# Kernel optimization log

Hardware: AMD Instinct MI355X
Metric: run time of the kernel (lower is better)

Reference implementation:

```python
import jax, jax.numpy as jnp
import numpy as np

B, C, H, W = 32, 256, 56, 56
EPS = 1e-5

def _bin_act(x):
    # ReActNet BinaryActivation: forward = sign(x), STE via piecewise polynomial
    out1 = jnp.where(x < -1.0, -1.0, x * x + 2.0 * x)
    out2 = jnp.where(x < 0.0, out1, -x * x + 2.0 * x)
    out3 = jnp.where(x < 1.0, out2, 1.0)
    return out3 + jax.lax.stop_gradient(jnp.sign(x) - out3)

def _bin_weight(w):
    # forward = sign(w) * mean(|w|) per out-channel; grad via clip(w,-1,1)
    scale = jnp.mean(jnp.abs(w), axis=(1, 2, 3), keepdims=True)
    bw = jnp.sign(w) * scale
    cl = jnp.clip(w, -1.0, 1.0)
    return cl + jax.lax.stop_gradient(bw - cl)

def _conv1x1(x, w):
    # x: [B,C,H,W], w: [P,C,1,1] -> [B,P,H,W]
    return jnp.einsum('bchw,pc->bphw', x, w[:, :, 0, 0])

def _shift(x, k):
    # chunk channels into 4, roll H+k, H-k, W+k, W-k (circular, as torch.roll)
    x1, x2, x3, x4 = jnp.split(x, 4, axis=1)
    return jnp.concatenate([
        jnp.roll(x1, k, axis=2), jnp.roll(x2, -k, axis=2),
        jnp.roll(x3, k, axis=3), jnp.roll(x4, -k, axis=3)], axis=1)

def setup_inputs() -> dict:
    key = jax.random.key(0)
    ks = jax.random.split(key, 8)
    return {
        'x': jax.random.normal(ks[0], (B, C, H, W), dtype=jnp.float32),
        'bias0': jax.random.normal(ks[1], (C,), dtype=jnp.float32) * 0.1,
        'w1': jax.random.normal(ks[2], (C, C, 1, 1), dtype=jnp.float32) * 0.05,
        'w2': jax.random.normal(ks[3], (C, C, 1, 1), dtype=jnp.float32) * 0.05,
        'w3': jax.random.normal(ks[4], (C, C, 1, 1), dtype=jnp.float32) * 0.05,
        'gamma': jnp.ones((C,), dtype=jnp.float32),
        'beta': jnp.zeros((C,), dtype=jnp.float32),
        'bias1': jax.random.normal(ks[5], (C,), dtype=jnp.float32) * 0.1,
        'alpha': jnp.full((C,), 0.25, dtype=jnp.float32),  # PReLU init
        'bias2': jax.random.normal(ks[6], (C,), dtype=jnp.float32) * 0.1,
    }

def reference(x, bias0, w1, w2, w3, gamma, beta, bias1, alpha, bias2):
    ch = lambda v: v[None, :, None, None]
    residual = x
    out = x + ch(bias0)                      # move0 (LearnableBias)
    a = _bin_act(out)                        # binary activation (sign, STE)
    o1 = _conv1x1(a, _bin_weight(w1))        # binary_conv
    o2 = _conv1x1(_shift(a, 1), _bin_weight(w2))   # Shift + binary_conv1
    o3 = _conv1x1(_shift(a, 3), _bin_weight(w3))   # GlobalShift + binary_conv2
    s = o1 + o2 + o3
    # BatchNorm (training mode: batch statistics over B,H,W)
    mean = jnp.mean(s, axis=(0, 2, 3))
    var = jnp.var(s, axis=(0, 2, 3))
    h = (s - ch(mean)) * jax.lax.rsqrt(ch(var) + EPS) * ch(gamma) + ch(beta)
    h = h + residual                          # residual add
    h = h + ch(bias1)                         # move1
    h = jnp.where(h >= 0, h, ch(alpha) * h)   # PReLU
    h = h + ch(bias2)                         # move2
    return h
```

## Files before the change

kernel.cpp:

```cpp
#include <hip/hip_runtime.h>

typedef unsigned int u32;
typedef int i32x4 __attribute__((ext_vector_type(4)));
typedef float f32x4 __attribute__((ext_vector_type(4)));

#define HWP  3136
#define NPOS 100352
#define NMBLK 1568

#define ACT_OFF 0ull
#define ACT_BYTES (25690112ull)
#define W8_OFF  (ACT_OFF + ACT_BYTES)
#define W8_BYTES (196608ull)
#define SC_OFF  (W8_OFF + W8_BYTES)
#define SC_BYTES (3072ull)
#define PS_OFF  (SC_OFF + SC_BYTES)
#define PS_BYTES (256ull * NMBLK * 4)
#define PQ_OFF  (PS_OFF + PS_BYTES)
#define PQ_BYTES (256ull * NMBLK * 4)
#define PAR_OFF (PQ_OFF + PQ_BYTES)

__global__ __launch_bounds__(64) void k_pack_w(
    const float* __restrict__ w1, const float* __restrict__ w2,
    const float* __restrict__ w3, signed char* __restrict__ w8,
    float* __restrict__ scales) {
  int bid = blockIdx.x;
  int conv = bid >> 8, p = bid & 255;
  const float* w = (conv == 0) ? w1 : (conv == 1) ? w2 : w3;
  int lane = threadIdx.x;
  float asum = 0.0f;
#pragma unroll
  for (int k = 0; k < 4; ++k) {
    float v = w[p * 256 + k * 64 + lane];
    asum += fabsf(v);
    w8[(size_t)(conv * 256 + p) * 256 + k * 64 + lane] =
        (v > 0.0f) ? (signed char)1 : (signed char)-1;
  }
#pragma unroll
  for (int off = 32; off > 0; off >>= 1) asum += __shfl_down(asum, off);
  if (lane == 0) scales[conv * 256 + p] = asum * (1.0f / 256.0f);
}

__global__ __launch_bounds__(256) void k_pack_a(
    const float* __restrict__ x, const float* __restrict__ bias0,
    i32x4* __restrict__ act16) {
  int pos = blockIdx.x * 256 + threadIdx.x;
  int b = pos / HWP;
  int hw = pos - b * HWP;
  const float* xp = x + (size_t)b * 256 * HWP + hw;
  i32x4* op = act16 + (size_t)pos * 16;
#pragma unroll 2
  for (int c16 = 0; c16 < 16; ++c16) {
    i32x4 vv;
#pragma unroll
    for (int q = 0; q < 4; ++q) {
      u32 bb = 0;
#pragma unroll
      for (int cc = 0; cc < 4; ++cc) {
        int c = c16 * 16 + q * 4 + cc;
        float v = xp[(size_t)c * HWP] + bias0[c];
        bb |= (u32)((v > 0.0f) ? 0x01u : 0xFFu) << (cc * 8);
      }
      vv[q] = (int)bb;
    }
    op[c16] = vv;
  }
}

__device__ __forceinline__ void compute_s(
    int m, int n0, const signed char* __restrict__ act,
    const signed char* __restrict__ w8, const float* __restrict__ scales,
    signed char* lds, f32x4 (&sout)[4]) {
  const int tid = threadIdx.x;
  const int lane = tid & 63, wid = tid >> 6;
  const int l15 = lane & 15, l4 = lane >> 4;
  const int ch = n0 + wid * 16 + l15;

  i32x4 bfrag[3][4];
#pragma unroll
  for (int conv = 0; conv < 3; ++conv)
#pragma unroll
    for (int ks = 0; ks < 4; ++ks)
      bfrag[conv][ks] = *(const i32x4*)(w8 + (size_t)(conv * 256 + ch) * 256 +
                                        ks * 64 + l4 * 16);
  float sc0 = scales[ch], sc1 = scales[256 + ch], sc2 = scales[512 + ch];

  int bimg = m / 49;
  int hw0 = (m - bimg * 49) * 64;
  for (int id = tid; id < 3072; id += 512) {
    int tile = id >> 10;
    int rem = id & 1023;
    int row = rem >> 4;
    int c16 = rem & 15;
    int grp = c16 >> 2;
    int hw = hw0 + row;
    int h = hw / 56, w = hw - h * 56;
    int sh = h, sw = w;
    if (tile == 1) {
      if (grp == 0)      sh = (h == 0) ? 55 : h - 1;
      else if (grp == 1) sh = (h == 55) ? 0 : h + 1;
      else if (grp == 2) sw = (w == 0) ? 55 : w - 1;
      else               sw = (w == 55) ? 0 : w + 1;
    } else if (tile == 2) {
      if (grp == 0)      sh = (h < 3) ? h + 53 : h - 3;
      else if (grp == 1) sh = (h >= 53) ? h - 53 : h + 3;
      else if (grp == 2) sw = (w < 3) ? w + 53 : w - 3;
      else               sw = (w >= 53) ? w - 53 : w + 3;
    }
    size_t spos = (size_t)(bimg * HWP + sh * 56 + sw);
    i32x4 v = *(const i32x4*)(act + spos * 256 + c16 * 16);
    *(i32x4*)(lds + tile * 16384 + row * 256 + ((c16 ^ (row & 7)) << 4)) = v;
  }
  __syncthreads();

#pragma unroll
  for (int msub = 0; msub < 4; ++msub) {
    int row = msub * 16 + l15;
    int rx = row & 7;
    i32x4 acc0 = {0, 0, 0, 0}, acc1 = {0, 0, 0, 0}, acc2 = {0, 0, 0, 0};
#pragma unroll
    for (int ks = 0; ks < 4; ++ks) {
      int off = row * 256 + (((ks * 4 + l4) ^ rx) << 4);
      i32x4 a0 = *(const i32x4*)(lds + off);
      i32x4 a1 = *(const i32x4*)(lds + 16384 + off);
      i32x4 a2 = *(const i32x4*)(lds + 32768 + off);
      acc0 = __builtin_amdgcn_mfma_i32_16x16x64_i8(a0, bfrag[0][ks], acc0, 0, 0, 0);
      acc1 = __builtin_amdgcn_mfma_i32_16x16x64_i8(a1, bfrag[1][ks], acc1, 0, 0, 0);
      acc2 = __builtin_amdgcn_mfma_i32_16x16x64_i8(a2, bfrag[2][ks], acc2, 0, 0, 0);
    }
    f32x4 s;
#pragma unroll
    for (int r = 0; r < 4; ++r)
      s[r] = sc0 * (float)acc0[r] + sc1 * (float)acc1[r] + sc2 * (float)acc2[r];
    sout[msub] = s;
  }
}

__global__ __launch_bounds__(512) void k_stats2(
    const signed char* __restrict__ act, const signed char* __restrict__ w8,
    const float* __restrict__ scales, float* __restrict__ ps,
    float* __restrict__ pq) {
  __shared__ alignas(16) signed char lds[49152];
  int m = blockIdx.x, n0 = blockIdx.y * 128;
  f32x4 s[4];
  compute_s(m, n0, act, w8, scales, lds, s);
  float ss = 0.0f, sq = 0.0f;
#pragma unroll
  for (int msub = 0; msub < 4; ++msub)
#pragma unroll
    for (int r = 0; r < 4; ++r) {
      ss += s[msub][r];
      sq = fmaf(s[msub][r], s[msub][r], sq);
    }
  ss += __shfl_xor(ss, 16); sq += __shfl_xor(sq, 16);
  ss += __shfl_xor(ss, 32); sq += __shfl_xor(sq, 32);
  int lane = threadIdx.x & 63, wid = threadIdx.x >> 6;
  if ((lane >> 4) == 0) {
    int ch = n0 + wid * 16 + lane;
    ps[(size_t)ch * NMBLK + m] = ss;
    pq[(size_t)ch * NMBLK + m] = sq;
  }
}

__global__ __launch_bounds__(256) void k_bn(
    const float* __restrict__ ps, const float* __restrict__ pq,
    const float* __restrict__ gamma, const float* __restrict__ beta,
    const float* __restrict__ bias1, float* __restrict__ par) {
  int ch = blockIdx.x;
  int tid = threadIdx.x;
  double as = 0.0, aq = 0.0;
  for (int i = tid; i < NMBLK; i += 256) {
    as += (double)ps[(size_t)ch * NMBLK + i];
    aq += (double)pq[(size_t)ch * NMBLK + i];
  }
  __shared__ double sd0[256], sd1[256];
  sd0[tid] = as; sd1[tid] = aq;
  __syncthreads();
  for (int s = 128; s > 0; s >>= 1) {
    if (tid < s) { sd0[tid] += sd0[tid + s]; sd1[tid] += sd1[tid + s]; }
    __syncthreads();
  }
  if (tid == 0) {
    double mean = sd0[0] * (1.0 / NPOS);
    double var = sd1[0] * (1.0 / NPOS) - mean * mean;
    float mm = (float)((double)gamma[ch] / sqrt(var + 1e-5));
    par[ch] = mm;
    par[256 + ch] = beta[ch] + bias1[ch] - (float)mean * mm;
  }
}

__global__ __launch_bounds__(512) void k_out2(
    const signed char* __restrict__ act, const signed char* __restrict__ w8,
    const float* __restrict__ scales, const float* __restrict__ par,
    const float* __restrict__ alpha, const float* __restrict__ bias2,
    const float* __restrict__ x, float* __restrict__ out) {
  __shared__ alignas(16) signed char lds[49152];
  int m = blockIdx.x, n0 = blockIdx.y * 128;
  f32x4 s[4];
  compute_s(m, n0, act, w8, scales, lds, s);
  int tid = threadIdx.x, lane = tid & 63, wid = tid >> 6;
  int l15 = lane & 15, l4 = lane >> 4;
  int ch = n0 + wid * 16 + l15;
  float mul = par[ch], add = par[256 + ch], al = alpha[ch], b2 = bias2[ch];
  int bimg = m / 49;
  int hw0 = (m - bimg * 49) * 64;
  size_t base = ((size_t)bimg * 256 + ch) * HWP + hw0 + l4 * 4;
#pragma unroll
  for (int msub = 0; msub < 4; ++msub) {
    f32x4 xv = *(const f32x4*)(x + base + msub * 16);
    f32x4 o;
#pragma unroll
    for (int r = 0; r < 4; ++r) {
      float t = fmaf(s[msub][r], mul, add) + xv[r];
      t = (t >= 0.0f) ? t : al * t;
      o[r] = t + b2;
    }
    *(f32x4*)(out + base + msub * 16) = o;
  }
}

extern "C" void kernel_launch(void* const* d_in, const int* in_sizes, int n_in,
                              void* d_out, int out_size, void* d_ws,
                              size_t ws_size, hipStream_t stream) {
  const float* x     = (const float*)d_in[0];
  const float* bias0 = (const float*)d_in[1];
  const float* w1    = (const float*)d_in[2];
  const float* w2    = (const float*)d_in[3];
  const float* w3    = (const float*)d_in[4];
  const float* gamma = (const float*)d_in[5];
  const float* beta  = (const float*)d_in[6];
  const float* bias1 = (const float*)d_in[7];
  const float* alpha = (const float*)d_in[8];
  const float* bias2 = (const float*)d_in[9];
  float* out = (float*)d_out;

  char* ws = (char*)d_ws;
  signed char* act = (signed char*)(ws + ACT_OFF);
  i32x4* act16     = (i32x4*)(ws + ACT_OFF);
  signed char* w8  = (signed char*)(ws + W8_OFF);
  float* scales    = (float*)(ws + SC_OFF);
  float* ps        = (float*)(ws + PS_OFF);
  float* pq        = (float*)(ws + PQ_OFF);
  float* par       = (float*)(ws + PAR_OFF);

  hipLaunchKernelGGL(k_pack_w, dim3(768), dim3(64), 0, stream, w1, w2, w3, w8,
                     scales);
  hipLaunchKernelGGL(k_pack_a, dim3(392), dim3(256), 0, stream, x, bias0,
                     act16);
  hipLaunchKernelGGL(k_stats2, dim3(NMBLK, 2), dim3(512), 0, stream, act, w8,
                     scales, ps, pq);
  hipLaunchKernelGGL(k_bn, dim3(256), dim3(256), 0, stream, ps, pq, gamma,
                     beta, bias1, par);
  hipLaunchKernelGGL(k_out2, dim3(NMBLK, 2), dim3(512), 0, stream, act, w8,
                     scales, par, alpha, bias2, x, out);
}
```

Before: 370.1 us.

## Load shifted activation fragments directly from global in channel-block-major layout, drop LDS staging

Packed activations are now stored channel-block-major ([16][NPOS] of 16-byte vectors), so each lane gathers its MFMA A-fragments for the unshifted and shifted positions straight from global memory. This removes the LDS tile, its swizzle and the __syncthreads. The cost is that all 8 waves redundantly read the same activation rows, relying on L1/L2 hits. A block-index swizzle (swz_m) is added to change which spatial tiles run together, aiming for better cache locality across concurrently scheduled blocks.

```diff
diff --git a/kernel.cpp b/kernel.cpp
--- a/kernel.cpp
+++ b/kernel.cpp
@@ -48,7 +48,6 @@
   int b = pos / HWP;
   int hw = pos - b * HWP;
   const float* xp = x + (size_t)b * 256 * HWP + hw;
-  i32x4* op = act16 + (size_t)pos * 16;
 #pragma unroll 2
   for (int c16 = 0; c16 < 16; ++c16) {
     i32x4 vv;
@@ -63,14 +62,28 @@
       }
       vv[q] = (int)bb;
     }
-    op[c16] = vv;
-  }
+    act16[(size_t)c16 * NPOS + pos] = vv;
+  }
+}
+
+__device__ __forceinline__ void neighbor_pos(int row, int base, int (&p9)[9]) {
+  int h = row / 56;
+  int w = row - h * 56;
+  p9[0] = base + row;
+  int hm1 = (h == 0) ? 55 : h - 1, hp1 = (h == 55) ? 0 : h + 1;
+  int wm1 = (w == 0) ? 55 : w - 1, wp1 = (w == 55) ? 0 : w + 1;
+  int hm3 = (h < 3) ? h + 53 : h - 3, hp3 = (h >= 53) ? h - 53 : h + 3;
+  int wm3 = (w < 3) ? w + 53 : w - 3, wp3 = (w >= 53) ? w - 53 : w + 3;
+  p9[1] = base + hm1 * 56 + w;  p9[2] = base + hp1 * 56 + w;
+  p9[3] = base + h * 56 + wm1;  p9[4] = base + h * 56 + wp1;
+  p9[5] = base + hm3 * 56 + w;  p9[6] = base + hp3 * 56 + w;
+  p9[7] = base + h * 56 + wm3;  p9[8] = base + h * 56 + wp3;
 }
 
 __device__ __forceinline__ void compute_s(
-    int m, int n0, const signed char* __restrict__ act,
+    int m, int n0, const i32x4* __restrict__ act16,
     const signed char* __restrict__ w8, const float* __restrict__ scales,
-    signed char* lds, f32x4 (&sout)[4]) {
+    f32x4 (&sout)[4]) {
   const int tid = threadIdx.x;
   const int lane = tid & 63, wid = tid >> 6;
   const int l15 = lane & 15, l4 = lane >> 4;
@@ -87,46 +100,27 @@
 
   int bimg = m / 49;
   int hw0 = (m - bimg * 49) * 64;
-  for (int id = tid; id < 3072; id += 512) {
-    int tile = id >> 10;
-    int rem = id & 1023;
-    int row = rem >> 4;
-    int c16 = rem & 15;
-    int grp = c16 >> 2;
-    int hw = hw0 + row;
-    int h = hw / 56, w = hw - h * 56;
-    int sh = h, sw = w;
-    if (tile == 1) {
-      if (grp == 0)      sh = (h == 0) ? 55 : h - 1;
-      else if (grp == 1) sh = (h == 55) ? 0 : h + 1;
-      else if (grp == 2) sw = (w == 0) ? 55 : w - 1;
-      else               sw = (w == 55) ? 0 : w + 1;
-    } else if (tile == 2) {
-      if (grp == 0)      sh = (h < 3) ? h + 53 : h - 3;
-      else if (grp == 1) sh = (h >= 53) ? h - 53 : h + 3;
-      else if (grp == 2) sw = (w < 3) ? w + 53 : w - 3;
-      else               sw = (w >= 53) ? w - 53 : w + 3;
-    }
-    size_t spos = (size_t)(bimg * HWP + sh * 56 + sw);
-    i32x4 v = *(const i32x4*)(act + spos * 256 + c16 * 16);
-    *(i32x4*)(lds + tile * 16384 + row * 256 + ((c16 ^ (row & 7)) << 4)) = v;
-  }
-  __syncthreads();
+  int base = bimg * HWP;
 
 #pragma unroll
   for (int msub = 0; msub < 4; ++msub) {
-    int row = msub * 16 + l15;
-    int rx = row & 7;
+    int row = hw0 + msub * 16 + l15;
+    int p9[9];
+    neighbor_pos(row, base, p9);
     i32x4 acc0 = {0, 0, 0, 0}, acc1 = {0, 0, 0, 0}, acc2 = {0, 0, 0, 0};
+    i32x4 a0[4], a1[4], a2[4];
 #pragma unroll
     for (int ks = 0; ks < 4; ++ks) {
-      int off = row * 256 + (((ks * 4 + l4) ^ rx) << 4);
-      i32x4 a0 = *(const i32x4*)(lds + off);
-      i32x4 a1 = *(const i32x4*)(lds + 16384 + off);
-      i32x4 a2 = *(const i32x4*)(lds + 32768 + off);
-      acc0 = __builtin_amdgcn_mfma_i32_16x16x64_i8(a0, bfrag[0][ks], acc0, 0, 0, 0);
-      acc1 = __builtin_amdgcn_mfma_i32_16x16x64_i8(a1, bfrag[1][ks], acc1, 0, 0, 0);
-      acc2 = __builtin_amdgcn_mfma_i32_16x16x64_i8(a2, bfrag[2][ks], acc2, 0, 0, 0);
+      const i32x4* cb = act16 + (size_t)(ks * 4 + l4) * NPOS;
+      a0[ks] = cb[p9[0]];
+      a1[ks] = cb[p9[1 + ks]];
+      a2[ks] = cb[p9[5 + ks]];
+    }
+#pragma unroll
+    for (int ks = 0; ks < 4; ++ks) {
+      acc0 = __builtin_amdgcn_mfma_i32_16x16x64_i8(a0[ks], bfrag[0][ks], acc0, 0, 0, 0);
+      acc1 = __builtin_amdgcn_mfma_i32_16x16x64_i8(a1[ks], bfrag[1][ks], acc1, 0, 0, 0);
+      acc2 = __builtin_amdgcn_mfma_i32_16x16x64_i8(a2[ks], bfrag[2][ks], acc2, 0, 0, 0);
     }
     f32x4 s;
 #pragma unroll
@@ -136,14 +130,17 @@
   }
 }
 
+__device__ __forceinline__ int swz_m(int bid) {
+  return (bid & 7) * 196 + (bid >> 3);
+}
+
 __global__ __launch_bounds__(512) void k_stats2(
-    const signed char* __restrict__ act, const signed char* __restrict__ w8,
+    const i32x4* __restrict__ act16, const signed char* __restrict__ w8,
     const float* __restrict__ scales, float* __restrict__ ps,
     float* __restrict__ pq) {
-  __shared__ alignas(16) signed char lds[49152];
-  int m = blockIdx.x, n0 = blockIdx.y * 128;
+  int m = swz_m(blockIdx.x), n0 = blockIdx.y * 128;
   f32x4 s[4];
-  compute_s(m, n0, act, w8, scales, lds, s);
+  compute_s(m, n0, act16, w8, scales, s);
   float ss = 0.0f, sq = 0.0f;
 #pragma unroll
   for (int msub = 0; msub < 4; ++msub)
@@ -190,14 +187,13 @@
 }
 
 __global__ __launch_bounds__(512) void k_out2(
-    const signed char* __restrict__ act, const signed char* __restrict__ w8,
+    const i32x4* __restrict__ act16, const signed char* __restrict__ w8,
     const float* __restrict__ scales, const float* __restrict__ par,
     const float* __restrict__ alpha, const float* __restrict__ bias2,
     const float* __restrict__ x, float* __restrict__ out) {
-  __shared__ alignas(16) signed char lds[49152];
-  int m = blockIdx.x, n0 = blockIdx.y * 128;
+  int m = swz_m(blockIdx.x), n0 = blockIdx.y * 128;
   f32x4 s[4];
-  compute_s(m, n0, act, w8, scales, lds, s);
+  compute_s(m, n0, act16, w8, scales, s);
   int tid = threadIdx.x, lane = tid & 63, wid = tid >> 6;
   int l15 = lane & 15, l4 = lane >> 4;
   int ch = n0 + wid * 16 + l15;
@@ -235,7 +231,6 @@
   float* out = (float*)d_out;
 
   char* ws = (char*)d_ws;
-  signed char* act = (signed char*)(ws + ACT_OFF);
   i32x4* act16     = (i32x4*)(ws + ACT_OFF);
   signed char* w8  = (signed char*)(ws + W8_OFF);
   float* scales    = (float*)(ws + SC_OFF);
@@ -247,10 +242,10 @@
                      scales);
   hipLaunchKernelGGL(k_pack_a, dim3(392), dim3(256), 0, stream, x, bias0,
                      act16);
-  hipLaunchKernelGGL(k_stats2, dim3(NMBLK, 2), dim3(512), 0, stream, act, w8,
-                     scales, ps, pq);
+  hipLaunchKernelGGL(k_stats2, dim3(NMBLK, 2), dim3(512), 0, stream, act16,
+                     w8, scales, ps, pq);
   hipLaunchKernelGGL(k_bn, dim3(256), dim3(256), 0, stream, ps, pq, gamma,
                      beta, bias1, par);
-  hipLaunchKernelGGL(k_out2, dim3(NMBLK, 2), dim3(512), 0, stream, act, w8,
+  hipLaunchKernelGGL(k_out2, dim3(NMBLK, 2), dim3(512), 0, stream, act16, w8,
                      scales, par, alpha, bias2, x, out);
 }
```

New measurement: 359.5 us. 2.9% less time.
